# Kernel tuning notes

Hardware: AMD Instinct MI355X
Metric: run time of the kernel (lower is better)

The kernel has to match this reference:

```python
import jax, jax.numpy as jnp
import numpy as np

P = 2            # power (even positive int)
TEMPERATURE = 1.0
SCALE = 1.0 / np.sqrt(64.0)  # sqrt(head_dim) scaling
EPS = 1e-6


def setup_inputs() -> dict:
    key = jax.random.key(0)
    kq, kk, kv = jax.random.split(key, 3)
    shape = (4, 16, 2048, 64)  # (B, H, N, head_dim)
    return {
        "q": jax.random.normal(kq, shape, dtype=jnp.float32),
        "k": jax.random.normal(kk, shape, dtype=jnp.float32),
        "v": jax.random.normal(kv, shape, dtype=jnp.float32),
    }


def reference(q, k, v):
    # logits = q @ k^T * scale / temperature : (B, H, N, N)
    logits = jnp.einsum("bhnd,bhmd->bhnm", q, k) * (SCALE / TEMPERATURE)
    attn = logits ** P
    attn = attn / (attn.sum(axis=-1, keepdims=True) + EPS)
    return jnp.einsum("bhnm,bhmd->bhnd", attn, v)
```

## Files before the change

kernel.cpp:

```cpp
#include <hip/hip_runtime.h>

#define N_CTX 2048
#define DHEAD 64
#define SCALE_F 0.125f
#define EPS_F 1e-6f
#define KT 64
#define NITER (N_CTX / KT)
#define QBLK 256

typedef __attribute__((ext_vector_type(8))) short short8;
typedef __attribute__((ext_vector_type(4))) short short4v;
typedef __attribute__((ext_vector_type(4))) float float4v;
typedef __attribute__((ext_vector_type(2))) unsigned uint2v;
typedef __attribute__((ext_vector_type(4))) unsigned uint4v;

#if defined(__HIP_DEVICE_COMPILE__) && __has_builtin(__builtin_amdgcn_cvt_pk_bf16_f32)
typedef __attribute__((ext_vector_type(2))) __bf16 bf16x2;
__device__ __forceinline__ unsigned pack2(float a, float b) {
    union { bf16x2 v; unsigned u; } x;
    x.v = __builtin_amdgcn_cvt_pk_bf16_f32(a, b);
    return x.u;
}
#else
__device__ __forceinline__ unsigned bf1(float f) {
    union { float f; unsigned u; } x; x.f = f;
    return (x.u + 0x7FFFu + ((x.u >> 16) & 1u)) >> 16;
}
__device__ __forceinline__ unsigned pack2(float a, float b) {
    return bf1(a) | (bf1(b) << 16);
}
#endif

#if defined(__HIP_DEVICE_COMPILE__)
  #if __has_builtin(__builtin_amdgcn_mfma_f32_16x16x16bf16_1k)
    #define MFMA16(a, b, c) __builtin_amdgcn_mfma_f32_16x16x16bf16_1k(a, b, c, 0, 0, 0)
  #elif __has_builtin(__builtin_amdgcn_mfma_f32_16x16x16_bf16_1k)
    #define MFMA16(a, b, c) __builtin_amdgcn_mfma_f32_16x16x16_bf16_1k(a, b, c, 0, 0, 0)
  #else
    __device__ __forceinline__ float4v mfma16_asm(short4v a, short4v b, float4v c) {
        asm volatile("v_mfma_f32_16x16x16_bf16 %0, %1, %2, %0"
                     : "+v"(c) : "v"(a), "v"(b));
        return c;
    }
    #define MFMA16(a, b, c) mfma16_asm(a, b, c)
  #endif
#else
  #define MFMA16(a, b, c) (c)
#endif


__global__ __launch_bounds__(512, 4)
void powsm_attn(const float* __restrict__ qg, const float* __restrict__ kg,
                const float* __restrict__ vg, float* __restrict__ og)
{
    __shared__ short Ks[64][72];
    __shared__ short Vt[64][68];
    __shared__ float Dn[8][32];

    const int i     = blockIdx.x;
    const int bh    = (i & 7) * 8 + ((i >> 3) & 7);
    const int qtile = i >> 6;

    const int tid  = threadIdx.x;
    const int wave = tid >> 6;
    const int lane = tid & 63;
    const int qd   = lane >> 4;
    const int c    = lane & 15;

    const size_t base = (size_t)bh * N_CTX * DHEAD;
    const float* qp = qg + base;
    const float* kp = kg + base;
    const float* vp = vg + base;
    float*       op = og + base;

    const int qw0 = qtile * QBLK + wave * 32;

    short8 Qf[2][2];
    #pragma unroll
    for (int qt = 0; qt < 2; ++qt) {
        #pragma unroll
        for (int ks = 0; ks < 2; ++ks) {
            const float* src = qp + (size_t)(qw0 + qt*16 + c) * DHEAD + ks*32 + qd*8;
            float4v a = *(const float4v*)(src);
            float4v b = *(const float4v*)(src + 4);
            uint4v u;
            u[0] = pack2(a[0]*SCALE_F, a[1]*SCALE_F);
            u[1] = pack2(a[2]*SCALE_F, a[3]*SCALE_F);
            u[2] = pack2(b[0]*SCALE_F, b[1]*SCALE_F);
            u[3] = pack2(b[2]*SCALE_F, b[3]*SCALE_F);
            union { uint4v u; short8 s; } cv; cv.u = u;
            Qf[qt][ks] = cv.s;
        }
    }

    float4v Oacc[2][4];
    #pragma unroll
    for (int qt = 0; qt < 2; ++qt)
        #pragma unroll
        for (int nt = 0; nt < 4; ++nt)
            Oacc[qt][nt] = (float4v){0.f, 0.f, 0.f, 0.f};
    float4v dacc[2];
    dacc[0] = (float4v){0.f, 0.f, 0.f, 0.f};
    dacc[1] = (float4v){0.f, 0.f, 0.f, 0.f};

    const bool isV = (wave >= 4);
    const int  st  = tid & 255;
    const int  sr  = st >> 4;
    const int  sc  = st & 15;

    float4v pf[4];
    if (!isV) {
        #pragma unroll
        for (int u = 0; u < 4; ++u)
            pf[u] = *(const float4v*)(kp + (size_t)(sr + u*16) * DHEAD + sc*4);
    } else {
        #pragma unroll
        for (int j = 0; j < 4; ++j)
            pf[j] = *(const float4v*)(vp + (size_t)(4*sr + j) * DHEAD + sc*4);
    }

    #pragma unroll 1
    for (int kvi = 0; kvi < NITER; ++kvi) {
        __syncthreads();

        if (!isV) {
            #pragma unroll
            for (int u = 0; u < 4; ++u) {
                uint2v w; w[0] = pack2(pf[u][0], pf[u][1]); w[1] = pack2(pf[u][2], pf[u][3]);
                *(uint2v*)&Ks[sr + u*16][sc*4] = w;
            }
        } else {
            #pragma unroll
            for (int kk = 0; kk < 4; ++kk) {
                uint2v w; w[0] = pack2(pf[0][kk], pf[1][kk]); w[1] = pack2(pf[2][kk], pf[3][kk]);
                *(uint2v*)&Vt[4*sc + kk][4*sr] = w;
            }
        }
        __syncthreads();

        if (kvi + 1 < NITER) {
            const float* src = (isV ? vp : kp) + (size_t)(kvi + 1) * KT * DHEAD;
            if (!isV) {
                #pragma unroll
                for (int u = 0; u < 4; ++u)
                    pf[u] = *(const float4v*)(src + (size_t)(sr + u*16) * DHEAD + sc*4);
            } else {
                #pragma unroll
                for (int j = 0; j < 4; ++j)
                    pf[j] = *(const float4v*)(src + (size_t)(4*sr + j) * DHEAD + sc*4);
            }
        }

        #pragma unroll
        for (int mt = 0; mt < 4; ++mt) {
            float4v s[2];
            s[0] = (float4v){0.f, 0.f, 0.f, 0.f};
            s[1] = (float4v){0.f, 0.f, 0.f, 0.f};
            #pragma unroll
            for (int ks = 0; ks < 2; ++ks) {
                short8 af = *(const short8*)&Ks[mt*16 + c][ks*32 + qd*8];
                #pragma unroll
                for (int qt = 0; qt < 2; ++qt)
                    s[qt] = __builtin_amdgcn_mfma_f32_16x16x32_bf16(af, Qf[qt][ks], s[qt], 0, 0, 0);
            }
            short4v pa[2];
            #pragma unroll
            for (int qt = 0; qt < 2; ++qt) {
                float4v p = s[qt] * s[qt];
                dacc[qt] += p;
                union { uint2v u; short4v s; } cv;
                cv.u[0] = pack2(p[0], p[1]); cv.u[1] = pack2(p[2], p[3]);
                pa[qt] = cv.s;
            }
            #pragma unroll
            for (int nt = 0; nt < 4; ++nt) {
                short4v bf = *(const short4v*)&Vt[nt*16 + c][mt*16 + qd*4];
                #pragma unroll
                for (int qt = 0; qt < 2; ++qt)
                    Oacc[qt][nt] = MFMA16(pa[qt], bf, Oacc[qt][nt]);
            }
        }
    }

    #pragma unroll
    for (int qt = 0; qt < 2; ++qt) {
        float d = (dacc[qt][0] + dacc[qt][1]) + (dacc[qt][2] + dacc[qt][3]);
        d += __shfl_xor(d, 16);
        d += __shfl_xor(d, 32);
        if (qd == 0) Dn[wave][qt*16 + c] = d;
    }
    __syncthreads();

    #pragma unroll
    for (int qt = 0; qt < 2; ++qt) {
        #pragma unroll
        for (int r = 0; r < 4; ++r) {
            float inv = 1.0f / (Dn[wave][qt*16 + qd*4 + r] + EPS_F);
            float* dst = op + (size_t)(qw0 + qt*16 + qd*4 + r) * DHEAD + c;
            #pragma unroll
            for (int nt = 0; nt < 4; ++nt)
                dst[nt*16] = Oacc[qt][nt][r] * inv;
        }
    }
}

extern "C" void kernel_launch(void* const* d_in, const int* in_sizes, int n_in,
                              void* d_out, int out_size, void* d_ws, size_t ws_size,
                              hipStream_t stream) {
    const float* q = (const float*)d_in[0];
    const float* k = (const float*)d_in[1];
    const float* v = (const float*)d_in[2];
    float* out = (float*)d_out;
    dim3 grid((N_CTX / QBLK) * 64, 1, 1);
    powsm_attn<<<grid, dim3(512, 1, 1), 0, stream>>>(q, k, v, out);
}
```

Baseline: 210.9 us.

## Double-buffer K/V tiles in LDS with 256-thread blocks and one barrier per step

```diff
diff --git a/kernel.cpp b/kernel.cpp
--- a/kernel.cpp
+++ b/kernel.cpp
@@ -6,7 +6,7 @@
 #define EPS_F 1e-6f
 #define KT 64
 #define NITER (N_CTX / KT)
-#define QBLK 256
+#define QBLK 128
 
 typedef __attribute__((ext_vector_type(8))) short short8;
 typedef __attribute__((ext_vector_type(4))) short short4v;
@@ -49,13 +49,13 @@
 #endif
 
 
-__global__ __launch_bounds__(512, 4)
+__global__ __launch_bounds__(256, 3)
 void powsm_attn(const float* __restrict__ qg, const float* __restrict__ kg,
                 const float* __restrict__ vg, float* __restrict__ og)
 {
-    __shared__ short Ks[64][72];
-    __shared__ short Vt[64][68];
-    __shared__ float Dn[8][32];
+    __shared__ short Ks[2][64][72];
+    __shared__ short Vt[2][64][68];
+    __shared__ float Dn[4][32];
 
     const int i     = blockIdx.x;
     const int bh    = (i & 7) * 8 + ((i >> 3) & 7);
@@ -103,53 +103,50 @@
     dacc[0] = (float4v){0.f, 0.f, 0.f, 0.f};
     dacc[1] = (float4v){0.f, 0.f, 0.f, 0.f};
 
-    const bool isV = (wave >= 4);
-    const int  st  = tid & 255;
-    const int  sr  = st >> 4;
-    const int  sc  = st & 15;
-
-    float4v pf[4];
-    if (!isV) {
-        #pragma unroll
-        for (int u = 0; u < 4; ++u)
-            pf[u] = *(const float4v*)(kp + (size_t)(sr + u*16) * DHEAD + sc*4);
-    } else {
-        #pragma unroll
-        for (int j = 0; j < 4; ++j)
-            pf[j] = *(const float4v*)(vp + (size_t)(4*sr + j) * DHEAD + sc*4);
-    }
+    const int sr = tid >> 4;
+    const int sc = tid & 15;
+
+    float4v pK[4], pV[4];
+
+    #define LOAD_TILE(t)                                                        \
+        do {                                                                    \
+            const float* kn_ = kp + (size_t)(t) * KT * DHEAD;                   \
+            const float* vn_ = vp + (size_t)(t) * KT * DHEAD;                   \
+            _Pragma("unroll")                                                   \
+            for (int u_ = 0; u_ < 4; ++u_)                                      \
+                pK[u_] = *(const float4v*)(kn_ + (size_t)(sr + u_*16) * DHEAD + sc*4); \
+            _Pragma("unroll")                                                   \
+            for (int j_ = 0; j_ < 4; ++j_)                                      \
+                pV[j_] = *(const float4v*)(vn_ + (size_t)(4*sr + j_) * DHEAD + sc*4);  \
+        } while (0)
+
+    #define STAGE_TILE(buf)                                                     \
+        do {                                                                    \
+            _Pragma("unroll")                                                   \
+            for (int u_ = 0; u_ < 4; ++u_) {                                    \
+                uint2v w_; w_[0] = pack2(pK[u_][0], pK[u_][1]);                 \
+                           w_[1] = pack2(pK[u_][2], pK[u_][3]);                 \
+                *(uint2v*)&Ks[buf][sr + u_*16][sc*4] = w_;                      \
+            }                                                                   \
+            _Pragma("unroll")                                                   \
+            for (int kk_ = 0; kk_ < 4; ++kk_) {                                 \
+                uint2v w_; w_[0] = pack2(pV[0][kk_], pV[1][kk_]);               \
+                           w_[1] = pack2(pV[2][kk_], pV[3][kk_]);               \
+                *(uint2v*)&Vt[buf][4*sc + kk_][4*sr] = w_;                      \
+            }                                                                   \
+        } while (0)
+
+    LOAD_TILE(0);
+    STAGE_TILE(0);
+    LOAD_TILE(1);
+    __syncthreads();
 
     #pragma unroll 1
     for (int kvi = 0; kvi < NITER; ++kvi) {
-        __syncthreads();
-
-        if (!isV) {
-            #pragma unroll
-            for (int u = 0; u < 4; ++u) {
-                uint2v w; w[0] = pack2(pf[u][0], pf[u][1]); w[1] = pack2(pf[u][2], pf[u][3]);
-                *(uint2v*)&Ks[sr + u*16][sc*4] = w;
-            }
-        } else {
-            #pragma unroll
-            for (int kk = 0; kk < 4; ++kk) {
-                uint2v w; w[0] = pack2(pf[0][kk], pf[1][kk]); w[1] = pack2(pf[2][kk], pf[3][kk]);
-                *(uint2v*)&Vt[4*sc + kk][4*sr] = w;
-            }
-        }
-        __syncthreads();
-
-        if (kvi + 1 < NITER) {
-            const float* src = (isV ? vp : kp) + (size_t)(kvi + 1) * KT * DHEAD;
-            if (!isV) {
-                #pragma unroll
-                for (int u = 0; u < 4; ++u)
-                    pf[u] = *(const float4v*)(src + (size_t)(sr + u*16) * DHEAD + sc*4);
-            } else {
-                #pragma unroll
-                for (int j = 0; j < 4; ++j)
-                    pf[j] = *(const float4v*)(src + (size_t)(4*sr + j) * DHEAD + sc*4);
-            }
-        }
+        const int cur = kvi & 1;
+
+        if (kvi + 1 < NITER) STAGE_TILE(cur ^ 1);
+        if (kvi + 2 < NITER) LOAD_TILE(kvi + 2);
 
         #pragma unroll
         for (int mt = 0; mt < 4; ++mt) {
@@ -158,7 +155,7 @@
             s[1] = (float4v){0.f, 0.f, 0.f, 0.f};
             #pragma unroll
             for (int ks = 0; ks < 2; ++ks) {
-                short8 af = *(const short8*)&Ks[mt*16 + c][ks*32 + qd*8];
+                short8 af = *(const short8*)&Ks[cur][mt*16 + c][ks*32 + qd*8];
                 #pragma unroll
                 for (int qt = 0; qt < 2; ++qt)
                     s[qt] = __builtin_amdgcn_mfma_f32_16x16x32_bf16(af, Qf[qt][ks], s[qt], 0, 0, 0);
@@ -174,12 +171,13 @@
             }
             #pragma unroll
             for (int nt = 0; nt < 4; ++nt) {
-                short4v bf = *(const short4v*)&Vt[nt*16 + c][mt*16 + qd*4];
+                short4v bf = *(const short4v*)&Vt[cur][nt*16 + c][mt*16 + qd*4];
                 #pragma unroll
                 for (int qt = 0; qt < 2; ++qt)
                     Oacc[qt][nt] = MFMA16(pa[qt], bf, Oacc[qt][nt]);
             }
         }
+        __syncthreads();
     }
 
     #pragma unroll
@@ -212,5 +210,5 @@
     const float* v = (const float*)d_in[2];
     float* out = (float*)d_out;
     dim3 grid((N_CTX / QBLK) * 64, 1, 1);
-    powsm_attn<<<grid, dim3(512, 1, 1), 0, stream>>>(q, k, v, out);
-}
+    powsm_attn<<<grid, dim3(256, 1, 1), 0, stream>>>(q, k, v, out);
+}
```

Result: slower. 217.2 us (+3.0%).
